# Kernel tuning notes

Measured on AMD Instinct MI355X. Metric: run time of the kernel, lower is better.

## Reference

```python
import jax, jax.numpy as jnp
import numpy as np

B = 4
D = H = W = 128
N = 500_000
CIN = 32
COUT = 32
K = 5
EPS = 1e-4


def setup_inputs() -> dict:
    # unique voxel coordinates (submanifold sparse tensor sites)
    rng = np.random.default_rng(0)
    flat = rng.choice(B * D * H * W, size=N, replace=False)
    b = flat // (D * H * W)
    rem = flat % (D * H * W)
    z = rem // (H * W)
    rem2 = rem % (H * W)
    y = rem2 // W
    x = rem2 % W
    coords = jnp.asarray(np.stack([b, z, y, x], axis=1).astype(np.int32))  # [N,4]

    key = jax.random.key(0)
    k1, k2, k3, k4 = jax.random.split(key, 4)
    features = jax.random.normal(k1, (N, CIN), jnp.float32)
    gamma = 1.0 + 0.1 * jax.random.normal(k2, (CIN,), jnp.float32)
    beta = 0.1 * jax.random.normal(k3, (CIN,), jnp.float32)
    weight = jax.random.normal(k4, (K ** 3, CIN, COUT), jnp.float32) / np.sqrt(K ** 3 * CIN)
    return {"features": features, "coords": coords, "gamma": gamma, "beta": beta, "weight": weight}


def _subm_conv(feats, coords, weight):
    # dense site-index grid: flat voxel id -> row in feats (-1 if inactive)
    flat_idx = ((coords[:, 0] * D + coords[:, 1]) * H + coords[:, 2]) * W + coords[:, 3]
    grid = jnp.full((B * D * H * W,), -1, jnp.int32).at[flat_idx].set(
        jnp.arange(N, dtype=jnp.int32))

    r = jnp.arange(-(K // 2), K // 2 + 1, dtype=jnp.int32)
    offs = jnp.stack(jnp.meshgrid(r, r, r, indexing="ij"), axis=-1).reshape(-1, 3)  # [125,3] (dz,dy,dx)
    bounds = jnp.array([D, H, W], jnp.int32)

    def body(acc, off_w):
        off, w = off_w
        nb = coords[:, 1:] + off  # [N,3]
        inb = jnp.all((nb >= 0) & (nb < bounds), axis=1)
        nflat = ((coords[:, 0] * D + nb[:, 0]) * H + nb[:, 1]) * W + nb[:, 2]
        nidx = jnp.where(inb, grid[jnp.clip(nflat, 0, B * D * H * W - 1)], -1)
        valid = nidx >= 0
        g = jnp.where(valid[:, None], feats[jnp.clip(nidx, 0, N - 1)], 0.0)  # [N,CIN]
        return acc + g @ w, None

    acc, _ = jax.lax.scan(body, jnp.zeros((N, COUT), feats.dtype), (offs, weight))
    return acc


def reference(features, coords, gamma, beta, weight):
    # BatchNorm1d over active sites (training-mode batch stats, biased var)
    mean = jnp.mean(features, axis=0)
    var = jnp.mean(jnp.square(features - mean), axis=0)
    xhat = (features - mean) * jax.lax.rsqrt(var + EPS)
    y = jax.nn.relu(xhat * gamma + beta)
    # submanifold sparse 3D conv, kernel 5, padding 2, no bias
    return _subm_conv(y, coords, weight)
```

## Files before the change

kernel.cpp:

```cpp
#include <hip/hip_runtime.h>

typedef unsigned short u16;
typedef unsigned int u32;
typedef unsigned long long u64;

#define N_SITES 500000
#define CIN 32
#define COUT 32
#define DD 128
#define HHH 128
#define WWW 128
#define KVOL 125
#define EPSV 1e-4f
#define NVOX (4*DD*HHH*WWW)
#define RED_BLOCKS 504
#define CNT_BLOCKS 8192
#define NSLOT 500224
#define ZROW  N_SITES
#define SENTI (NVOX+4)

typedef short v8s __attribute__((ext_vector_type(8)));
typedef float v16f __attribute__((ext_vector_type(16)));

__device__ __forceinline__ u16 f2bf(float f){
  union { float f; u32 i; } v; v.f = f;
  u32 r = v.i + 0x7fffu + ((v.i >> 16) & 1u);
  return (u16)(r >> 16);
}

__launch_bounds__(256)
__global__ void bn_reduce(const float* __restrict__ x, float* __restrict__ partial){
  __shared__ float ssum[8][32], ssq[8][32];
  int tid = threadIdx.x;
  int c   = tid & 31;
  int row = tid >> 5;
  float s = 0.f, q = 0.f;
  for(int site = blockIdx.x*8 + row; site < N_SITES; site += gridDim.x*8){
    float f = x[(size_t)site*32 + c];
    s += f; q += f*f;
  }
  ssum[row][c] = s; ssq[row][c] = q;
  __syncthreads();
  if(tid < 32){
    float ts = 0.f, tq = 0.f;
    #pragma unroll
    for(int r = 0; r < 8; r++){ ts += ssum[r][tid]; tq += ssq[r][tid]; }
    partial[blockIdx.x*64 + tid]      = ts;
    partial[blockIdx.x*64 + 32 + tid] = tq;
  }
}

__global__ void bn_finalize_pad(const float* __restrict__ partial, const float* __restrict__ gamma,
                                const float* __restrict__ beta, float* __restrict__ ss, int nblk,
                                int* __restrict__ perm, u32* __restrict__ yzero){
  __shared__ float red[8][64];
  int tid = threadIdx.x;
  int c = tid & 31, r = tid >> 5;
  float s = 0.f, q = 0.f;
  for(int b = r; b < nblk; b += 8){
    s += partial[b*64 + c];
    q += partial[b*64 + 32 + c];
  }
  red[r][c] = s; red[r][32 + c] = q;
  __syncthreads();
  if(tid < 32){
    float ts = 0.f, tq = 0.f;
    #pragma unroll
    for(int rr = 0; rr < 8; rr++){ ts += red[rr][tid]; tq += red[rr][32 + tid]; }
    float mean = ts / (float)N_SITES;
    float var  = tq / (float)N_SITES - mean*mean;
    float scale = gamma[tid] * rsqrtf(var + EPSV);
    ss[tid]      = scale;
    ss[32 + tid] = beta[tid] - mean*scale;
  }
  if(tid < NSLOT - N_SITES) perm[N_SITES + tid] = perm[0];
  if(tid < 16) yzero[tid] = 0;
}

__launch_bounds__(256)
__global__ void bn_apply_y(const float4* __restrict__ xv, const float* __restrict__ ss,
                           const int* __restrict__ rank, uint4* __restrict__ yv){
  __shared__ float sc[64];
  int tid = threadIdx.x;
  if(tid < 64) sc[tid] = ss[tid];
  __syncthreads();
  const int total = N_SITES*CIN/8;
  int stride = gridDim.x*256;
  for(int i = blockIdx.x*256 + tid; i < total; i += stride){
    int c0 = (i & 3) * 8;
    int slot = rank[i >> 2];
    float4 a = xv[2*i], b = xv[2*i+1];
    float f[8] = {a.x,a.y,a.z,a.w,b.x,b.y,b.z,b.w};
    #pragma unroll
    for(int j = 0; j < 8; j++) f[j] = fmaxf(f[j]*sc[c0+j] + sc[32+c0+j], 0.f);
    uint4 o;
    o.x = ((u32)f2bf(f[1])<<16) | f2bf(f[0]);
    o.y = ((u32)f2bf(f[3])<<16) | f2bf(f[2]);
    o.z = ((u32)f2bf(f[5])<<16) | f2bf(f[4]);
    o.w = ((u32)f2bf(f[7])<<16) | f2bf(f[6]);
    yv[slot*4 + (i & 3)] = o;
  }
}

__launch_bounds__(256)
__global__ void build_grid(const int4* __restrict__ coords, int* __restrict__ grid){
  int i = blockIdx.x*256 + threadIdx.x;
  if(i >= N_SITES) return;
  int4 c = coords[i];
  grid[((c.x*DD + c.y)*HHH + c.z)*WWW + c.w] = i;
}

__launch_bounds__(256)
__global__ void count_blocks(const int* __restrict__ grid, int* __restrict__ blockcnt){
  int b = blockIdx.x, t = threadIdx.x;
  int cnt = 0;
  #pragma unroll
  for(int k = 0; k < 4; k++) cnt += (grid[b*1024 + k*256 + t] >= 0);
  #pragma unroll
  for(int o = 32; o > 0; o >>= 1) cnt += __shfl_down(cnt, o);
  __shared__ int wsum[4];
  if((t & 63) == 0) wsum[t >> 6] = cnt;
  __syncthreads();
  if(t == 0) blockcnt[b] = wsum[0] + wsum[1] + wsum[2] + wsum[3];
}

__launch_bounds__(1024)
__global__ void scan_blocks(const int* __restrict__ blockcnt, int* __restrict__ blockoff){
  __shared__ int wsum[16];
  int t = threadIdx.x;
  int lane = t & 63, w = t >> 6;
  int loc[8]; int v = 0;
  #pragma unroll
  for(int k = 0; k < 8; k++){ loc[k] = blockcnt[t*8 + k]; v += loc[k]; }
  int s = v;
  #pragma unroll
  for(int o = 1; o < 64; o <<= 1){
    int u = __shfl_up(s, o);
    if(lane >= o) s += u;
  }
  if(lane == 63) wsum[w] = s;
  __syncthreads();
  if(w == 0 && lane < 16){
    int x = wsum[lane];
    #pragma unroll
    for(int o = 1; o < 16; o <<= 1){
      int u = __shfl_up(x, o);
      if(lane >= o) x += u;
    }
    wsum[lane] = x;
  }
  __syncthreads();
  int base = s - v + (w > 0 ? wsum[w - 1] : 0);
  #pragma unroll
  for(int k = 0; k < 8; k++){ blockoff[t*8 + k] = base; base += loc[k]; }
}

__launch_bounds__(256)
__global__ void fill_perm(int* __restrict__ grid, const int* __restrict__ blockoff,
                          int* __restrict__ perm, int* __restrict__ rank){
  int b = blockIdx.x, t = threadIdx.x;
  int w = t >> 6, lane = t & 63;
  __shared__ int wcnt[4];
  __shared__ int carry;
  if(t == 0) carry = 0;
  __syncthreads();
  int base = blockoff[b];
  for(int p = 0; p < 4; p++){
    int v = b*1024 + p*256 + t;
    int s = grid[v];
    bool act = (s >= 0);
    u64 bal = __ballot(act);
    int pre = (int)__popcll(bal & ((1ull << lane) - 1ull));
    if(lane == 0) wcnt[w] = (int)__popcll(bal);
    __syncthreads();
    int woff = 0;
    for(int ww = 0; ww < w; ww++) woff += wcnt[ww];
    if(act){
      int slot = base + carry + woff + pre;
      perm[slot] = s;
      rank[s] = slot;
      grid[v] = slot;
    }
    int tot = wcnt[0] + wcnt[1] + wcnt[2] + wcnt[3];
    __syncthreads();
    if(t == 0) carry += tot;
    __syncthreads();
  }
}

__launch_bounds__(256)
__global__ void prep_wfrag(const float* __restrict__ w, u16* __restrict__ wf){
  int i = blockIdx.x*256 + threadIdx.x;
  if(i >= KVOL*2*64*8) return;
  int j    = i & 7;
  int lane = (i >> 3) & 63;
  int half = (i >> 9) & 1;
  int off  = i >> 10;
  int k = half*16 + ((lane >> 5) << 3) + j;
  int n = lane & 31;
  wf[i] = f2bf(w[off*1024 + k*32 + n]);
}

__launch_bounds__(256, 4)
__global__ void conv_mfma(const u16* __restrict__ y, const int4* __restrict__ coords,
                          const u16* __restrict__ wf, const int* __restrict__ gridp,
                          const int* __restrict__ perm, float* __restrict__ out){
  const char* __restrict__ yc  = (const char*)y;
  const char* __restrict__ gcp = (const char*)gridp;
  const v8s*  __restrict__ wfv8 = (const v8s*)wf;

  int t = threadIdx.x;
  int l = t & 63;
  int r31 = l & 31;
  int h = l >> 5;
  u32 koff = (u32)h << 4;

  int nwg = gridDim.x, bid = blockIdx.x;
  int xcd = bid & 7, rk = bid >> 3;
  int q8 = nwg >> 3, r8 = nwg & 7;
  int swz = (xcd < r8 ? xcd*(q8+1) : r8*(q8+1) + (xcd - r8)*q8) + rk;

  int slot = swz*256 + t;
  int p = perm[slot];
  int4 c = coords[p];
  int Z = c.y, Y = c.z, X = c.w;
  int base = ((c.x*DD + Z)*HHH + Y)*WWW + X;

  int b0 = __shfl(base, r31);
  int b1 = __shfl(base, 32 + r31);
  int x0 = __shfl(X, r31),  x1 = __shfl(X, 32 + r31);
  int y0 = __shfl(Y, r31),  y1 = __shfl(Y, 32 + r31);
  int z0 = __shfl(Z, r31),  z1 = __shfl(Z, 32 + r31);

  bool okx0[5], okx1[5], oky0[5], oky1[5];
  #pragma unroll
  for(int k = 0; k < 5; k++){
    okx0[k] = (u32)(x0 + k - 2) < WWW;
    okx1[k] = (u32)(x1 + k - 2) < WWW;
    oky0[k] = (u32)(y0 + k - 2) < HHH;
    oky1[k] = (u32)(y1 + k - 2) < HHH;
  }

  v16f acc0, acc1;
  #pragma unroll
  for(int i = 0; i < 16; i++){ acc0[i] = 0.f; acc1[i] = 0.f; }

  const int HW = HHH*WWW;

#define PROBE_WIN(rr) { \
    bool zy0 = okz0 && oky0[rr]; \
    bool zy1 = okz1 && oky1[rr]; \
    int st0 = zy0 ? (pb0 + ((rr)-2)*WWW - 2) : SENTI; \
    int st1 = zy1 ? (pb1 + ((rr)-2)*WWW - 2) : SENTI; \
    int al0 = st0 & ~3, al1 = st1 & ~3; \
    sh0 = st0 - al0; sh1 = st1 - al1; \
    rA0 = *(const int4*)(gcp + (long)al0*4); \
    rA1 = *(const int4*)(gcp + (long)al0*4 + 16); \
    rB0 = *(const int4*)(gcp + (long)al1*4); \
    rB1 = *(const int4*)(gcp + (long)al1*4 + 16); \
  }

#define EXTRACT(rr) { \
    int e0[8] = {rA0.x,rA0.y,rA0.z,rA0.w,rA1.x,rA1.y,rA1.z,rA1.w}; \
    int e1[8] = {rB0.x,rB0.y,rB0.z,rB0.w,rB1.x,rB1.y,rB1.z,rB1.w}; \
    bool sa2 = (sh0 & 2) != 0, sa1 = (sh0 & 1) != 0; \
    bool sb2 = (sh1 & 2) != 0, sb1 = (sh1 & 1) != 0; \
    _Pragma("unroll") \
    for(int k = 0; k < 5; k++){ \
      int t0 = sa2 ? e0[k+2] : e0[k]; \
      int t1 = sa2 ? e0[k+3] : e0[k+1]; \
      nvA[k] = okx0[k] ? (sa1 ? t1 : t0) : -1; \
      int u0 = sb2 ? e1[k+2] : e1[k]; \
      int u1 = sb2 ? e1[k+3] : e1[k+1]; \
      nvB[k] = okx1[k] ? (sb1 ? u1 : u0) : -1; \
    } \
  }

  #pragma unroll 1
  for(int dz = -2; dz <= 2; dz++){
    bool okz0 = (u32)(z0 + dz) < DD;
    bool okz1 = (u32)(z1 + dz) < DD;
    int pb0 = b0 + dz*HW, pb1 = b1 + dz*HW;

    int4 rA0, rA1, rB0, rB1;
    int sh0, sh1;
    PROBE_WIN(0)
    asm volatile("" ::: "memory");

    #pragma unroll
    for(int r = 0; r < 5; r++){
      const v8s* wrow = wfv8 + (u32)(((dz + 2)*5 + r)*5) * 128u;
      v8s wb[10];
      #pragma unroll
      for(int k = 0; k < 5; k++){
        wb[k*2+0] = wrow[k*128 + l];
        wb[k*2+1] = wrow[k*128 + 64 + l];
      }
      int nvA[5], nvB[5];
      EXTRACT(r)
      v8s fr[20];
      #pragma unroll
      for(int k = 0; k < 5; k++){
        u32 n0 = (u32)nvA[k], n1 = (u32)nvB[k];
        u32 rw0 = n0 < (u32)ZROW ? n0 : (u32)ZROW;
        u32 rw1 = n1 < (u32)ZROW ? n1 : (u32)ZROW;
        u32 ya0 = (rw0 << 6) + koff;
        u32 ya1 = (rw1 << 6) + koff;
        fr[k*4+0] = *(const v8s*)(yc + ya0);
        fr[k*4+1] = *(const v8s*)(yc + ya0 + 32u);
        fr[k*4+2] = *(const v8s*)(yc + ya1);
        fr[k*4+3] = *(const v8s*)(yc + ya1 + 32u);
      }
      asm volatile("" ::: "memory");
      if(r < 4){
        PROBE_WIN(r+1)
        asm volatile("" ::: "memory");
      }
      #pragma unroll
      for(int k = 0; k < 5; k++){
        acc0 = __builtin_amdgcn_mfma_f32_32x32x16_bf16(fr[k*4+0], wb[k*2+0], acc0, 0, 0, 0);
        acc0 = __builtin_amdgcn_mfma_f32_32x32x16_bf16(fr[k*4+1], wb[k*2+1], acc0, 0, 0, 0);
        acc1 = __builtin_amdgcn_mfma_f32_32x32x16_bf16(fr[k*4+2], wb[k*2+0], acc1, 0, 0, 0);
        acc1 = __builtin_amdgcn_mfma_f32_32x32x16_bf16(fr[k*4+3], wb[k*2+1], acc1, 0, 0, 0);
      }
    }
  }
#undef PROBE_WIN
#undef EXTRACT

  #pragma unroll
  for(int rg = 0; rg < 16; rg++){
    int row = (rg & 3) + ((rg >> 2) << 3) + (h << 2);
    int s0 = __shfl(p, row);
    int s1 = __shfl(p, 32 + row);
    out[(size_t)s0*32 + r31] = acc0[rg];
    out[(size_t)s1*32 + r31] = acc1[rg];
  }
}

extern "C" void kernel_launch(void* const* d_in, const int* in_sizes, int n_in,
                              void* d_out, int out_size, void* d_ws, size_t ws_size,
                              hipStream_t stream) {
  const float* feats  = (const float*)d_in[0];
  const int4*  coords = (const int4*) d_in[1];
  const float* gamma  = (const float*)d_in[2];
  const float* beta   = (const float*)d_in[3];
  const float* wght   = (const float*)d_in[4];
  float* out = (float*)d_out;

  char* ws = (char*)d_ws;
  int*   grid_raw = (int*)  ws;
  int*   gridp    = grid_raw + 8;
  u16*   yperm    = (u16*)  (ws + 33554560);
  u16*   wf       = (u16*)  (ws + 65554624);
  int*   perm     = (int*)  (ws + 65810624);
  int*   blockcnt = (int*)  (ws + 67811520);
  int*   blockoff = (int*)  (ws + 67844288);
  float* partial  = (float*)(ws + 67877056);
  float* ss       = (float*)(ws + 68006080);
  int* rank = (int*)d_out;

  hipMemsetAsync(grid_raw, 0xFF, (size_t)(NVOX+32)*4, stream);

  build_grid  <<<(N_SITES+255)/256, 256, 0, stream>>>(coords, gridp);
  count_blocks<<<CNT_BLOCKS, 256, 0, stream>>>(gridp, blockcnt);
  scan_blocks <<<1, 1024, 0, stream>>>(blockcnt, blockoff);
  fill_perm   <<<CNT_BLOCKS, 256, 0, stream>>>(gridp, blockoff, perm, rank);

  bn_reduce      <<<RED_BLOCKS, 256, 0, stream>>>(feats, partial);
  bn_finalize_pad<<<1, 256, 0, stream>>>(partial, gamma, beta, ss, RED_BLOCKS,
                                         perm, (u32*)(yperm + (size_t)ZROW*32));
  bn_apply_y <<<2048, 256, 0, stream>>>((const float4*)feats, ss, rank, (uint4*)yperm);

  prep_wfrag<<<(KVOL*2*64*8 + 255)/256, 256, 0, stream>>>(wght, wf);

  conv_mfma<<<NSLOT/256, 256, 0, stream>>>(yperm, coords, wf, gridp, perm, out);
}
```

Measured before the change: 464.0 us.

## Fuse block counting into grid build and stage conv weights in LDS

The separate count_blocks pass over the dense voxel grid is removed. build_grid now increments a per-1024-voxel counter with atomicAdd, and the counters are zeroed by an extra memset. The conv kernel moves to 512-thread blocks and copies each dz-plane's bf16 weight fragments (about 51 KB) into shared memory between barriers, so MFMA weight operands come from LDS instead of repeated global loads. The trade-offs are 500k global atomics, two block-wide syncs per dz iteration, and larger LDS use that can limit the number of resident blocks per CU.

```diff
diff --git a/kernel.cpp b/kernel.cpp
--- a/kernel.cpp
+++ b/kernel.cpp
@@ -103,25 +103,14 @@
 }
 
 __launch_bounds__(256)
-__global__ void build_grid(const int4* __restrict__ coords, int* __restrict__ grid){
+__global__ void build_grid(const int4* __restrict__ coords, int* __restrict__ grid,
+                           int* __restrict__ blockcnt){
   int i = blockIdx.x*256 + threadIdx.x;
   if(i >= N_SITES) return;
   int4 c = coords[i];
-  grid[((c.x*DD + c.y)*HHH + c.z)*WWW + c.w] = i;
-}
-
-__launch_bounds__(256)
-__global__ void count_blocks(const int* __restrict__ grid, int* __restrict__ blockcnt){
-  int b = blockIdx.x, t = threadIdx.x;
-  int cnt = 0;
-  #pragma unroll
-  for(int k = 0; k < 4; k++) cnt += (grid[b*1024 + k*256 + t] >= 0);
-  #pragma unroll
-  for(int o = 32; o > 0; o >>= 1) cnt += __shfl_down(cnt, o);
-  __shared__ int wsum[4];
-  if((t & 63) == 0) wsum[t >> 6] = cnt;
-  __syncthreads();
-  if(t == 0) blockcnt[b] = wsum[0] + wsum[1] + wsum[2] + wsum[3];
+  int v = ((c.x*DD + c.y)*HHH + c.z)*WWW + c.w;
+  grid[v] = i;
+  atomicAdd(&blockcnt[v >> 10], 1);
 }
 
 __launch_bounds__(1024)
@@ -201,13 +190,13 @@
   wf[i] = f2bf(w[off*1024 + k*32 + n]);
 }
 
-__launch_bounds__(256, 4)
+__launch_bounds__(512)
 __global__ void conv_mfma(const u16* __restrict__ y, const int4* __restrict__ coords,
                           const u16* __restrict__ wf, const int* __restrict__ gridp,
                           const int* __restrict__ perm, float* __restrict__ out){
   const char* __restrict__ yc  = (const char*)y;
   const char* __restrict__ gcp = (const char*)gridp;
-  const v8s*  __restrict__ wfv8 = (const v8s*)wf;
+  __shared__ v8s swf[3200];
 
   int t = threadIdx.x;
   int l = t & 63;
@@ -220,7 +209,7 @@
   int q8 = nwg >> 3, r8 = nwg & 7;
   int swz = (xcd < r8 ? xcd*(q8+1) : r8*(q8+1) + (xcd - r8)*q8) + rk;
 
-  int slot = swz*256 + t;
+  int slot = swz*512 + t;
   int p = perm[slot];
   int4 c = coords[p];
   int Z = c.y, Y = c.z, X = c.w;
@@ -246,6 +235,7 @@
   for(int i = 0; i < 16; i++){ acc0[i] = 0.f; acc1[i] = 0.f; }
 
   const int HW = HHH*WWW;
+  const uint4* __restrict__ wfv = (const uint4*)wf;
 
 #define PROBE_WIN(rr) { \
     bool zy0 = okz0 && oky0[rr]; \
@@ -287,15 +277,22 @@
     PROBE_WIN(0)
     asm volatile("" ::: "memory");
 
+    __syncthreads();
+    {
+      u32 pbase = (u32)((dz + 2) * 3200);
+      #pragma unroll
+      for(int it = 0; it < 7; it++){
+        int ch = it*512 + t;
+        if(ch < 3200){
+          uint4 v = wfv[pbase + ch];
+          *(uint4*)&swf[ch] = v;
+        }
+      }
+    }
+    __syncthreads();
+
     #pragma unroll
     for(int r = 0; r < 5; r++){
-      const v8s* wrow = wfv8 + (u32)(((dz + 2)*5 + r)*5) * 128u;
-      v8s wb[10];
-      #pragma unroll
-      for(int k = 0; k < 5; k++){
-        wb[k*2+0] = wrow[k*128 + l];
-        wb[k*2+1] = wrow[k*128 + 64 + l];
-      }
       int nvA[5], nvB[5];
       EXTRACT(r)
       v8s fr[20];
@@ -318,10 +315,13 @@
       }
       #pragma unroll
       for(int k = 0; k < 5; k++){
-        acc0 = __builtin_amdgcn_mfma_f32_32x32x16_bf16(fr[k*4+0], wb[k*2+0], acc0, 0, 0, 0);
-        acc0 = __builtin_amdgcn_mfma_f32_32x32x16_bf16(fr[k*4+1], wb[k*2+1], acc0, 0, 0, 0);
-        acc1 = __builtin_amdgcn_mfma_f32_32x32x16_bf16(fr[k*4+2], wb[k*2+0], acc1, 0, 0, 0);
-        acc1 = __builtin_amdgcn_mfma_f32_32x32x16_bf16(fr[k*4+3], wb[k*2+1], acc1, 0, 0, 0);
+        int o = r*5 + k;
+        v8s wb0 = swf[o*128 + l];
+        v8s wb1 = swf[o*128 + 64 + l];
+        acc0 = __builtin_amdgcn_mfma_f32_32x32x16_bf16(fr[k*4+0], wb0, acc0, 0, 0, 0);
+        acc0 = __builtin_amdgcn_mfma_f32_32x32x16_bf16(fr[k*4+1], wb1, acc0, 0, 0, 0);
+        acc1 = __builtin_amdgcn_mfma_f32_32x32x16_bf16(fr[k*4+2], wb0, acc1, 0, 0, 0);
+        acc1 = __builtin_amdgcn_mfma_f32_32x32x16_bf16(fr[k*4+3], wb1, acc1, 0, 0, 0);
       }
     }
   }
@@ -361,9 +361,9 @@
   int* rank = (int*)d_out;
 
   hipMemsetAsync(grid_raw, 0xFF, (size_t)(NVOX+32)*4, stream);
-
-  build_grid  <<<(N_SITES+255)/256, 256, 0, stream>>>(coords, gridp);
-  count_blocks<<<CNT_BLOCKS, 256, 0, stream>>>(gridp, blockcnt);
+  hipMemsetAsync(blockcnt, 0, 32768, stream);
+
+  build_grid  <<<(N_SITES+255)/256, 256, 0, stream>>>(coords, gridp, blockcnt);
   scan_blocks <<<1, 1024, 0, stream>>>(blockcnt, blockoff);
   fill_perm   <<<CNT_BLOCKS, 256, 0, stream>>>(gridp, blockoff, perm, rank);
 
@@ -374,5 +374,5 @@
 
   prep_wfrag<<<(KVOL*2*64*8 + 255)/256, 256, 0, stream>>>(wght, wf);
 
-  conv_mfma<<<NSLOT/256, 256, 0, stream>>>(yperm, coords, wf, gridp, perm, out);
-}
+  conv_mfma<<<NSLOT/512, 512, 0, stream>>>(yperm, coords, wf, gridp, perm, out);
+}
```

New measurement: 458.4 us. No clear change (-1.2%).
